# Performance work log

Measured on AMD Instinct MI355X. Metric: run time of the kernel, lower is better.

The kernel has to match this reference:

```python
import jax, jax.numpy as jnp
import numpy as np
import math

NUM_HEADS = 16

def setup_inputs() -> dict:
    key = jax.random.key(0)
    ks = jax.random.split(key, 5)
    d_model = 1024
    std = math.sqrt(2.0 / (d_model + d_model))
    x = jax.random.normal(ks[0], (2, 2048, d_model), dtype=jnp.float32)
    Wq = jax.random.normal(ks[1], (d_model, d_model), dtype=jnp.float32) * std
    Wk = jax.random.normal(ks[2], (d_model, d_model), dtype=jnp.float32) * std
    Wv = jax.random.normal(ks[3], (d_model, d_model), dtype=jnp.float32) * std
    Wo = jax.random.normal(ks[4], (d_model, d_model), dtype=jnp.float32) * std
    return {"x": x, "Wq": Wq, "Wk": Wk, "Wv": Wv, "Wo": Wo}

def reference(x, Wq, Wk, Wv, Wo):
    # x: [b, s, d]; W*: [d_out, d_in]
    b, s, d = x.shape
    h = NUM_HEADS
    dh = d // h
    def proj(W):
        y = jnp.einsum('bsd,ed->bse', x, W)           # [b, s, d]
        return y.reshape(b, s, h, dh).transpose(0, 2, 1, 3)  # [b, h, s, dh]
    Q, K, V = proj(Wq), proj(Wk), proj(Wv)
    scale = 1.0 / math.sqrt(dh)
    logits = jnp.einsum('bhqd,bhkd->bhqk', Q, K) * scale  # [b, h, s, s]
    causal = jnp.tril(jnp.ones((s, s), dtype=bool))
    logits = jnp.where(causal, logits, -jnp.inf)
    attn = jax.nn.softmax(logits, axis=-1)
    out = jnp.einsum('bhqk,bhkd->bhqd', attn, V)          # [b, h, s, dh]
    out = out.transpose(0, 2, 1, 3).reshape(b, s, d)
    return jnp.einsum('bsv,dv->bsd', out, Wo)
```

## Files before the change

kernel.cpp:

```cpp
#include <hip/hip_runtime.h>
#include <hip/hip_bf16.h>
#include <math.h>

typedef unsigned short ushort_t;
typedef __attribute__((ext_vector_type(8))) short bf16x8;
typedef __attribute__((ext_vector_type(4))) float f32x4;

#define MFMA16(a,b,c) __builtin_amdgcn_mfma_f32_16x16x32_bf16(a,b,c,0,0,0)
#define QSCALE 0.1803368801111204f

typedef unsigned int u32;
typedef __attribute__((address_space(1))) const u32* gp1_t;
typedef __attribute__((address_space(3))) u32* lp3_t;

__device__ __forceinline__ void async_copy16(void* l, const void* g) {
    __builtin_amdgcn_global_load_lds((gp1_t)g, (lp3_t)l, 16, 0, 0);
}

__device__ __forceinline__ ushort_t f2bf(float f) {
    unsigned u = __float_as_uint(f);
    unsigned r = u + 0x7fffu + ((u >> 16) & 1u);
    return (ushort_t)(r >> 16);
}

__global__ __launch_bounds__(256) void cvt_kernel(
    const float* __restrict__ x,  const float* __restrict__ wq,
    const float* __restrict__ wk, const float* __restrict__ wv,
    const float* __restrict__ wo, ushort_t* __restrict__ dst)
{
    size_t base = ((size_t)blockIdx.x * 256 + threadIdx.x) * 8;
    const float* src; size_t off;
    if      (base < 4194304ul) { src = x;  off = base; }
    else if (base < 5242880ul) { src = wq; off = base - 4194304ul; }
    else if (base < 6291456ul) { src = wk; off = base - 5242880ul; }
    else if (base < 7340032ul) { src = wv; off = base - 6291456ul; }
    else                       { src = wo; off = base - 7340032ul; }
    float4 a = *(const float4*)(src + off);
    float4 b = *(const float4*)(src + off + 4);
    struct alignas(16) U8 { ushort_t v[8]; } o;
    o.v[0]=f2bf(a.x); o.v[1]=f2bf(a.y); o.v[2]=f2bf(a.z); o.v[3]=f2bf(a.w);
    o.v[4]=f2bf(b.x); o.v[5]=f2bf(b.y); o.v[6]=f2bf(b.z); o.v[7]=f2bf(b.w);
    *(U8*)(dst + base) = o;
}

__global__ __launch_bounds__(512) void gemm_bt(
    const ushort_t* __restrict__ A, const ushort_t* __restrict__ B,
    ushort_t* __restrict__ Oq, ushort_t* __restrict__ Ok,
    ushort_t* __restrict__ Ovt, float* __restrict__ Of, int is_out)
{
    __shared__ ushort_t As[2][128 * 64];
    __shared__ ushort_t Bs[2][128 * 64];
    const int t = threadIdx.x, l = t & 63, w = t >> 6;
    const int l4 = l >> 4, lm = l & 15;
    const int wr = w >> 1, wc = w & 1;

    const int nwg = gridDim.x * gridDim.y;
    const int orig = (int)blockIdx.y * gridDim.x + (int)blockIdx.x;
    const int qq = nwg >> 3;
    const int swz = (orig & 7) * qq + (orig >> 3);
    const int n0 = (swz % gridDim.x) * 128;
    const int m0 = (swz / gridDim.x) * 128;

    const int srow = t >> 3, scol = t & 7;

    f32x4 acc[2][4] = {};

    #pragma unroll
    for (int i = 0; i < 2; ++i) {
        const int row = i * 64 + srow;
        const int c = scol ^ (row & 7);
        async_copy16((char*)&As[0][0] + i * 8192 + t * 16,
                     A + (size_t)(m0 + row) * 1024 + c * 8);
        async_copy16((char*)&Bs[0][0] + i * 8192 + t * 16,
                     B + (size_t)(n0 + row) * 1024 + c * 8);
    }

    for (int kt = 0; kt < 16; ++kt) {
        const int cur = kt & 1;
        if (kt + 1 < 16) {
            const int k0 = (kt + 1) * 64;
            #pragma unroll
            for (int i = 0; i < 2; ++i) {
                const int row = i * 64 + srow;
                const int c = scol ^ (row & 7);
                async_copy16((char*)&As[cur ^ 1][0] + i * 8192 + t * 16,
                             A + (size_t)(m0 + row) * 1024 + k0 + c * 8);
                async_copy16((char*)&Bs[cur ^ 1][0] + i * 8192 + t * 16,
                             B + (size_t)(n0 + row) * 1024 + k0 + c * 8);
            }
            asm volatile("s_waitcnt vmcnt(4)" ::: "memory");
        } else {
            asm volatile("s_waitcnt vmcnt(0)" ::: "memory");
        }
        __builtin_amdgcn_s_barrier();

        #pragma unroll
        for (int ks = 0; ks < 2; ++ks) {
            bf16x8 af[2], bfr[4];
            #pragma unroll
            for (int mi = 0; mi < 2; ++mi) {
                const int row = wr * 32 + mi * 16 + lm;
                const int ch = l4 + 4 * ks;
                af[mi] = *(const bf16x8*)(&As[cur][0] + row * 64 + ((ch ^ (row & 7)) << 3));
            }
            #pragma unroll
            for (int ni = 0; ni < 4; ++ni) {
                const int row = wc * 64 + ni * 16 + lm;
                const int ch = l4 + 4 * ks;
                bfr[ni] = *(const bf16x8*)(&Bs[cur][0] + row * 64 + ((ch ^ (row & 7)) << 3));
            }
            #pragma unroll
            for (int mi = 0; mi < 2; ++mi)
                #pragma unroll
                for (int ni = 0; ni < 4; ++ni)
                    acc[mi][ni] = MFMA16(af[mi], bfr[ni], acc[mi][ni]);
        }
        asm volatile("s_waitcnt lgkmcnt(0)" ::: "memory");
        __builtin_amdgcn_s_barrier();
    }

    const int mb = m0 + wr * 32, nb = n0 + wc * 64;
    if (is_out) {
        #pragma unroll
        for (int mi = 0; mi < 2; ++mi)
            #pragma unroll
            for (int ni = 0; ni < 4; ++ni) {
                const int n = nb + ni * 16 + lm;
                const int mr = mb + mi * 16 + l4 * 4;
                #pragma unroll
                for (int r = 0; r < 4; ++r)
                    Of[(size_t)(mr + r) * 1024 + n] = acc[mi][ni][r];
            }
    } else if (nb >= 2048) {
        #pragma unroll
        for (int mi = 0; mi < 2; ++mi)
            #pragma unroll
            for (int ni = 0; ni < 4; ++ni) {
                const int nv = nb - 2048 + ni * 16 + lm;
                const int m = mb + mi * 16 + l4 * 4;
                const int b = m >> 11, s = m & 2047, h = nv >> 6, d = nv & 63;
                ushort4 pk;
                pk.x = f2bf(acc[mi][ni][0]); pk.y = f2bf(acc[mi][ni][1]);
                pk.z = f2bf(acc[mi][ni][2]); pk.w = f2bf(acc[mi][ni][3]);
                *(ushort4*)(Ovt + (((size_t)(b * 16 + h) * 64 + d) * 2048 + s)) = pk;
            }
    } else {
        ushort_t* O = (nb < 1024) ? Oq : Ok;
        const float qs = (nb < 1024) ? (float)QSCALE : 1.0f;
        const int nbase = nb & 1023;
        #pragma unroll
        for (int mi = 0; mi < 2; ++mi)
            #pragma unroll
            for (int ni = 0; ni < 4; ++ni) {
                const int n = nbase + ni * 16 + lm;
                const int h = n >> 6, d = n & 63;
                #pragma unroll
                for (int r = 0; r < 4; ++r) {
                    const int m = mb + mi * 16 + l4 * 4 + r;
                    const int b = m >> 11, s = m & 2047;
                    O[((size_t)(b * 16 + h) * 2048 + s) * 64 + d] =
                        f2bf(acc[mi][ni][r] * qs);
                }
            }
    }
}

template<bool MASK>
__device__ __forceinline__ void attn_tile2(
    const ushort_t* Kbuf, const ushort_t* Vbuf, ushort_t* Pw,
    const bf16x8 (&qf)[2][2], const bf16x8 ones,
    f32x4 (&o)[2][4], f32x4 (&ol)[2],
    int kv0, int q0w, int l4, int lm)
{
    f32x4 sf[2][4] = {};
    #pragma unroll
    for (int ks = 0; ks < 2; ++ks)
        #pragma unroll
        for (int cf = 0; cf < 4; ++cf) {
            const int rowK = cf * 16 + lm;
            const int ch = l4 + 4 * ks;
            bf16x8 kf = *(const bf16x8*)(Kbuf + rowK * 64 + ((ch ^ (rowK & 7)) << 3));
            sf[0][cf] = MFMA16(kf, qf[0][ks], sf[0][cf]);
            sf[1][cf] = MFMA16(kf, qf[1][ks], sf[1][cf]);
        }

    #pragma unroll
    for (int qi = 0; qi < 2; ++qi) {
        const int qrow = q0w + qi * 16 + lm;
        #pragma unroll
        for (int cf = 0; cf < 4; ++cf) {
            f32x4 s = sf[qi][cf];
            if (MASK) {
                #pragma unroll
                for (int r = 0; r < 4; ++r)
                    if (kv0 + cf * 16 + l4 * 4 + r > qrow) s[r] = -30000.f;
            }
            float p0 = __builtin_amdgcn_exp2f(s[0]);
            float p1 = __builtin_amdgcn_exp2f(s[1]);
            float p2 = __builtin_amdgcn_exp2f(s[2]);
            float p3 = __builtin_amdgcn_exp2f(s[3]);
            __hip_bfloat162 b01 = __float22bfloat162_rn(make_float2(p0, p1));
            __hip_bfloat162 b23 = __float22bfloat162_rn(make_float2(p2, p3));
            uint2 pkv;
            __builtin_memcpy(&pkv.x, &b01, 4);
            __builtin_memcpy(&pkv.y, &b23, 4);
            *(uint2*)&Pw[(qi * 16 + lm) * 72 + cf * 16 + l4 * 4] = pkv;
        }
    }

    #pragma unroll
    for (int ks = 0; ks < 2; ++ks) {
        bf16x8 pf0 = *(const bf16x8*)&Pw[(0 * 16 + lm) * 72 + ks * 32 + l4 * 8];
        bf16x8 pf1 = *(const bf16x8*)&Pw[(1 * 16 + lm) * 72 + ks * 32 + l4 * 8];
        #pragma unroll
        for (int df = 0; df < 4; ++df) {
            const int rowV = df * 16 + lm;
            const int ch = l4 + 4 * ks;
            bf16x8 vf = *(const bf16x8*)(Vbuf + rowV * 64 + ((ch ^ (rowV & 7)) << 3));
            o[0][df] = MFMA16(vf, pf0, o[0][df]);
            o[1][df] = MFMA16(vf, pf1, o[1][df]);
        }
        ol[0] = MFMA16(ones, pf0, ol[0]);
        ol[1] = MFMA16(ones, pf1, ol[1]);
    }
}

__global__ __launch_bounds__(512) void attn_kernel(
    const ushort_t* __restrict__ Qg, const ushort_t* __restrict__ Kg,
    const ushort_t* __restrict__ Vtg, ushort_t* __restrict__ Og)
{
    __shared__ ushort_t smem[51200];
    ushort_t* Ksm = smem;
    ushort_t* Vsm = smem + 16384;
    ushort_t* Psm = smem + 32768;

    const int t = threadIdx.x, l = t & 63, w = t >> 6;
    const int l4 = l >> 4, lm = l & 15;
    const int kvg = w >> 2, qg = w & 3;
    const int bh = blockIdx.x;
    const int qt = 15 - (int)blockIdx.y;
    const int q0 = qt * 128, q0w = q0 + qg * 32;

    const ushort_t* Kbh = Kg + (size_t)bh * 2048 * 64;
    const ushort_t* Vbh = Vtg + (size_t)bh * 64 * 2048;

    bf16x8 qf[2][2];
    #pragma unroll
    for (int qi = 0; qi < 2; ++qi) {
        const ushort_t* qp = Qg + ((size_t)bh * 2048 + q0w + qi * 16 + lm) * 64 + l4 * 8;
        qf[qi][0] = *(const bf16x8*)qp;
        qf[qi][1] = *(const bf16x8*)(qp + 32);
    }
    bf16x8 ones;
    #pragma unroll
    for (int i = 0; i < 8; ++i) ones[i] = (short)0x3F80;

    f32x4 o[2][4] = {};
    f32x4 ol[2] = {};

    const int tg = t & 255;
    const int sr0 = tg >> 3, sc0 = tg & 7;
    const ushort_t* kp[2]; const ushort_t* vp[2];
    char* kd[2]; char* vd[2];
    #pragma unroll
    for (int i = 0; i < 2; ++i) {
        const int row = i * 32 + sr0;
        const int c = sc0 ^ (row & 7);
        kp[i] = Kbh + row * 64 + c * 8;
        vp[i] = Vbh + (size_t)row * 2048 + c * 8;
        kd[i] = (char*)Ksm + kvg * 16384 + i * 4096 + tg * 16;
        vd[i] = (char*)Vsm + kvg * 16384 + i * 4096 + tg * 16;
    }
    ushort_t* Pw = Psm + w * 2304;
    const ushort_t* Kgrp = Ksm + kvg * 8192;
    const ushort_t* Vgrp = Vsm + kvg * 8192;

    const int nst = qt + 1;
    {
        const int kv0p = kvg * 64;
        #pragma unroll
        for (int i = 0; i < 2; ++i) {
            async_copy16(kd[i], kp[i] + (size_t)kv0p * 64);
            async_copy16(vd[i], vp[i] + kv0p);
        }
    }

    for (int s = 0; s < nst; ++s) {
        const int cur = s & 1;
        if (s + 1 < nst) {
            const int kv0n = (2 * (s + 1) + kvg) * 64;
            #pragma unroll
            for (int i = 0; i < 2; ++i) {
                async_copy16(kd[i] + (cur ^ 1) * 8192, kp[i] + (size_t)kv0n * 64);
                async_copy16(vd[i] + (cur ^ 1) * 8192, vp[i] + kv0n);
            }
            asm volatile("s_waitcnt vmcnt(4)" ::: "memory");
        } else {
            asm volatile("s_waitcnt vmcnt(0)" ::: "memory");
        }
        __builtin_amdgcn_s_barrier();

        const int kv0 = (2 * s + kvg) * 64;
        if ((s + 1 < nst) || (q0w + 31 >= kv0)) {
            if (s + 1 < nst)
                attn_tile2<false>(Kgrp + cur * 4096, Vgrp + cur * 4096, Pw,
                                  qf, ones, o, ol, kv0, q0w, l4, lm);
            else
                attn_tile2<true>(Kgrp + cur * 4096, Vgrp + cur * 4096, Pw,
                                 qf, ones, o, ol, kv0, q0w, l4, lm);
        }
        asm volatile("s_waitcnt lgkmcnt(0)" ::: "memory");
        __builtin_amdgcn_s_barrier();
    }

    float* sc = (float*)smem;
    const int mb_ = (qg * 64 + l) * 35;
    if (kvg == 1) {
        #pragma unroll
        for (int qi = 0; qi < 2; ++qi) {
            #pragma unroll
            for (int df = 0; df < 4; ++df)
                #pragma unroll
                for (int r = 0; r < 4; ++r)
                    sc[mb_ + qi * 17 + df * 4 + r] = o[qi][df][r];
            sc[mb_ + qi * 17 + 16] = ol[qi][0];
        }
    }
    __syncthreads();
    if (kvg == 0) {
        const int b = bh >> 4, h = bh & 15;
        #pragma unroll
        for (int qi = 0; qi < 2; ++qi) {
            const float lB = sc[mb_ + qi * 17 + 16];
            const float inv = 1.f / (ol[qi][0] + lB);
            const int srow_o = q0w + qi * 16 + lm;
            #pragma unroll
            for (int df = 0; df < 4; ++df) {
                ushort4 pk4;
                float v0 = (o[qi][df][0] + sc[mb_ + qi * 17 + df * 4 + 0]) * inv;
                float v1 = (o[qi][df][1] + sc[mb_ + qi * 17 + df * 4 + 1]) * inv;
                float v2 = (o[qi][df][2] + sc[mb_ + qi * 17 + df * 4 + 2]) * inv;
                float v3 = (o[qi][df][3] + sc[mb_ + qi * 17 + df * 4 + 3]) * inv;
                pk4.x = f2bf(v0); pk4.y = f2bf(v1); pk4.z = f2bf(v2); pk4.w = f2bf(v3);
                *(ushort4*)&Og[((size_t)(b * 2048 + srow_o)) * 1024 + h * 64 + df * 16 + l4 * 4] = pk4;
            }
        }
    }
}

extern "C" void kernel_launch(void* const* d_in, const int* in_sizes, int n_in,
                              void* d_out, int out_size, void* d_ws, size_t ws_size,
                              hipStream_t stream)
{
    const float* x  = (const float*)d_in[0];
    const float* Wq = (const float*)d_in[1];
    const float* Wk = (const float*)d_in[2];
    const float* Wv = (const float*)d_in[3];
    const float* Wo = (const float*)d_in[4];

    ushort_t* ws  = (ushort_t*)d_ws;
    ushort_t* xb  = ws;
    ushort_t* wqb = ws + 4194304;
    ushort_t* wob = ws + 7340032;
    ushort_t* Qw  = ws + 8388608;
    ushort_t* Kw  = ws + 12582912;
    ushort_t* Vtw = ws + 16777216;
    ushort_t* Aow = ws + 20971520;

    cvt_kernel<<<4096, 256, 0, stream>>>(x, Wq, Wk, Wv, Wo, ws);
    gemm_bt<<<dim3(24, 32), 512, 0, stream>>>(xb, wqb, Qw, Kw, Vtw, nullptr, 0);
    attn_kernel<<<dim3(32, 16), 512, 0, stream>>>(Qw, Kw, Vtw, Aow);
    gemm_bt<<<dim3(8, 32), 512, 0, stream>>>(Aow, wob, nullptr, nullptr, nullptr,
                                             (float*)d_out, 1);
}
```

Before: 101.5 us.

## Single-buffer V loads inside the step and split P buffer per query half

```diff
diff --git a/kernel.cpp b/kernel.cpp
--- a/kernel.cpp
+++ b/kernel.cpp
@@ -165,81 +165,18 @@
     }
 }
 
-template<bool MASK>
-__device__ __forceinline__ void attn_tile2(
-    const ushort_t* Kbuf, const ushort_t* Vbuf, ushort_t* Pw,
-    const bf16x8 (&qf)[2][2], const bf16x8 ones,
-    f32x4 (&o)[2][4], f32x4 (&ol)[2],
-    int kv0, int q0w, int l4, int lm)
-{
-    f32x4 sf[2][4] = {};
-    #pragma unroll
-    for (int ks = 0; ks < 2; ++ks)
-        #pragma unroll
-        for (int cf = 0; cf < 4; ++cf) {
-            const int rowK = cf * 16 + lm;
-            const int ch = l4 + 4 * ks;
-            bf16x8 kf = *(const bf16x8*)(Kbuf + rowK * 64 + ((ch ^ (rowK & 7)) << 3));
-            sf[0][cf] = MFMA16(kf, qf[0][ks], sf[0][cf]);
-            sf[1][cf] = MFMA16(kf, qf[1][ks], sf[1][cf]);
-        }
-
-    #pragma unroll
-    for (int qi = 0; qi < 2; ++qi) {
-        const int qrow = q0w + qi * 16 + lm;
-        #pragma unroll
-        for (int cf = 0; cf < 4; ++cf) {
-            f32x4 s = sf[qi][cf];
-            if (MASK) {
-                #pragma unroll
-                for (int r = 0; r < 4; ++r)
-                    if (kv0 + cf * 16 + l4 * 4 + r > qrow) s[r] = -30000.f;
-            }
-            float p0 = __builtin_amdgcn_exp2f(s[0]);
-            float p1 = __builtin_amdgcn_exp2f(s[1]);
-            float p2 = __builtin_amdgcn_exp2f(s[2]);
-            float p3 = __builtin_amdgcn_exp2f(s[3]);
-            __hip_bfloat162 b01 = __float22bfloat162_rn(make_float2(p0, p1));
-            __hip_bfloat162 b23 = __float22bfloat162_rn(make_float2(p2, p3));
-            uint2 pkv;
-            __builtin_memcpy(&pkv.x, &b01, 4);
-            __builtin_memcpy(&pkv.y, &b23, 4);
-            *(uint2*)&Pw[(qi * 16 + lm) * 72 + cf * 16 + l4 * 4] = pkv;
-        }
-    }
-
-    #pragma unroll
-    for (int ks = 0; ks < 2; ++ks) {
-        bf16x8 pf0 = *(const bf16x8*)&Pw[(0 * 16 + lm) * 72 + ks * 32 + l4 * 8];
-        bf16x8 pf1 = *(const bf16x8*)&Pw[(1 * 16 + lm) * 72 + ks * 32 + l4 * 8];
-        #pragma unroll
-        for (int df = 0; df < 4; ++df) {
-            const int rowV = df * 16 + lm;
-            const int ch = l4 + 4 * ks;
-            bf16x8 vf = *(const bf16x8*)(Vbuf + rowV * 64 + ((ch ^ (rowV & 7)) << 3));
-            o[0][df] = MFMA16(vf, pf0, o[0][df]);
-            o[1][df] = MFMA16(vf, pf1, o[1][df]);
-        }
-        ol[0] = MFMA16(ones, pf0, ol[0]);
-        ol[1] = MFMA16(ones, pf1, ol[1]);
-    }
-}
-
 __global__ __launch_bounds__(512) void attn_kernel(
     const ushort_t* __restrict__ Qg, const ushort_t* __restrict__ Kg,
     const ushort_t* __restrict__ Vtg, ushort_t* __restrict__ Og)
 {
-    __shared__ ushort_t smem[51200];
-    ushort_t* Ksm = smem;
-    ushort_t* Vsm = smem + 16384;
-    ushort_t* Psm = smem + 32768;
+    __shared__ char smem[65536];
 
     const int t = threadIdx.x, l = t & 63, w = t >> 6;
     const int l4 = l >> 4, lm = l & 15;
     const int kvg = w >> 2, qg = w & 3;
     const int bh = blockIdx.x;
     const int qt = 15 - (int)blockIdx.y;
-    const int q0 = qt * 128, q0w = q0 + qg * 32;
+    const int q0w = qt * 128 + qg * 32;
 
     const ushort_t* Kbh = Kg + (size_t)bh * 2048 * 64;
     const ushort_t* Vbh = Vtg + (size_t)bh * 64 * 2048;
@@ -268,46 +205,132 @@
         const int c = sc0 ^ (row & 7);
         kp[i] = Kbh + row * 64 + c * 8;
         vp[i] = Vbh + (size_t)row * 2048 + c * 8;
-        kd[i] = (char*)Ksm + kvg * 16384 + i * 4096 + tg * 16;
-        vd[i] = (char*)Vsm + kvg * 16384 + i * 4096 + tg * 16;
-    }
-    ushort_t* Pw = Psm + w * 2304;
-    const ushort_t* Kgrp = Ksm + kvg * 8192;
-    const ushort_t* Vgrp = Vsm + kvg * 8192;
+        kd[i] = smem + kvg * 16384 + i * 4096 + tg * 16;
+        vd[i] = smem + 32768 + kvg * 8192 + i * 4096 + tg * 16;
+    }
+    const int pswz = (lm & 7) << 4;
+    char* Pw = smem + 49152 + w * 2048;
+    const ushort_t* Vgrp = (const ushort_t*)(smem + 32768 + kvg * 8192);
 
     const int nst = qt + 1;
     {
         const int kv0p = kvg * 64;
         #pragma unroll
-        for (int i = 0; i < 2; ++i) {
+        for (int i = 0; i < 2; ++i)
             async_copy16(kd[i], kp[i] + (size_t)kv0p * 64);
-            async_copy16(vd[i], vp[i] + kv0p);
-        }
     }
 
     for (int s = 0; s < nst; ++s) {
         const int cur = s & 1;
+        const int kv0 = (2 * s + kvg) * 64;
+        #pragma unroll
+        for (int i = 0; i < 2; ++i)
+            async_copy16(vd[i], vp[i] + kv0);
         if (s + 1 < nst) {
             const int kv0n = (2 * (s + 1) + kvg) * 64;
             #pragma unroll
-            for (int i = 0; i < 2; ++i) {
+            for (int i = 0; i < 2; ++i)
                 async_copy16(kd[i] + (cur ^ 1) * 8192, kp[i] + (size_t)kv0n * 64);
-                async_copy16(vd[i] + (cur ^ 1) * 8192, vp[i] + kv0n);
-            }
             asm volatile("s_waitcnt vmcnt(4)" ::: "memory");
         } else {
-            asm volatile("s_waitcnt vmcnt(0)" ::: "memory");
-        }
-        __builtin_amdgcn_s_barrier();
-
-        const int kv0 = (2 * s + kvg) * 64;
-        if ((s + 1 < nst) || (q0w + 31 >= kv0)) {
-            if (s + 1 < nst)
-                attn_tile2<false>(Kgrp + cur * 4096, Vgrp + cur * 4096, Pw,
-                                  qf, ones, o, ol, kv0, q0w, l4, lm);
-            else
-                attn_tile2<true>(Kgrp + cur * 4096, Vgrp + cur * 4096, Pw,
-                                 qf, ones, o, ol, kv0, q0w, l4, lm);
+            asm volatile("s_waitcnt vmcnt(2)" ::: "memory");
+        }
+        __builtin_amdgcn_s_barrier();
+
+        const bool active = (s + 1 < nst) || (q0w + 31 >= kv0);
+        const bool last = (s + 1 == nst);
+        const ushort_t* Kgrp = (const ushort_t*)(smem + kvg * 16384 + cur * 8192);
+
+        f32x4 sf[2][4];
+        if (active) {
+            #pragma unroll
+            for (int qi = 0; qi < 2; ++qi)
+                #pragma unroll
+                for (int cf = 0; cf < 4; ++cf) sf[qi][cf] = (f32x4){0,0,0,0};
+            #pragma unroll
+            for (int ks = 0; ks < 2; ++ks)
+                #pragma unroll
+                for (int cf = 0; cf < 4; ++cf) {
+                    const int rowK = cf * 16 + lm;
+                    const int ch = l4 + 4 * ks;
+                    bf16x8 kf = *(const bf16x8*)(Kgrp + rowK * 64 + ((ch ^ (rowK & 7)) << 3));
+                    sf[0][cf] = MFMA16(kf, qf[0][ks], sf[0][cf]);
+                    sf[1][cf] = MFMA16(kf, qf[1][ks], sf[1][cf]);
+                }
+            {
+                const int qrow = q0w + 0 * 16 + lm;
+                #pragma unroll
+                for (int cf = 0; cf < 4; ++cf) {
+                    f32x4 sv = sf[0][cf];
+                    if (last) {
+                        #pragma unroll
+                        for (int r = 0; r < 4; ++r)
+                            if (kv0 + cf * 16 + l4 * 4 + r > qrow) sv[r] = -30000.f;
+                    }
+                    float p0 = __builtin_amdgcn_exp2f(sv[0]);
+                    float p1 = __builtin_amdgcn_exp2f(sv[1]);
+                    float p2 = __builtin_amdgcn_exp2f(sv[2]);
+                    float p3 = __builtin_amdgcn_exp2f(sv[3]);
+                    __hip_bfloat162 b01 = __float22bfloat162_rn(make_float2(p0, p1));
+                    __hip_bfloat162 b23 = __float22bfloat162_rn(make_float2(p2, p3));
+                    uint2 pkv;
+                    __builtin_memcpy(&pkv.x, &b01, 4);
+                    __builtin_memcpy(&pkv.y, &b23, 4);
+                    *(uint2*)(Pw + ((lm * 128 + cf * 32 + l4 * 8) ^ pswz)) = pkv;
+                }
+            }
+        }
+        asm volatile("s_waitcnt vmcnt(2)" ::: "memory");
+        if (last) asm volatile("s_waitcnt vmcnt(0)" ::: "memory");
+        __builtin_amdgcn_s_barrier();
+
+        if (active) {
+            #pragma unroll
+            for (int ks = 0; ks < 2; ++ks) {
+                bf16x8 pf = *(const bf16x8*)(Pw + ((lm * 128 + ks * 64 + l4 * 16) ^ pswz));
+                #pragma unroll
+                for (int df = 0; df < 4; ++df) {
+                    const int rowV = df * 16 + lm;
+                    const int ch = l4 + 4 * ks;
+                    bf16x8 vf = *(const bf16x8*)(Vgrp + rowV * 64 + ((ch ^ (rowV & 7)) << 3));
+                    o[0][df] = MFMA16(vf, pf, o[0][df]);
+                }
+                ol[0] = MFMA16(ones, pf, ol[0]);
+            }
+            {
+                const int qrow = q0w + 1 * 16 + lm;
+                #pragma unroll
+                for (int cf = 0; cf < 4; ++cf) {
+                    f32x4 sv = sf[1][cf];
+                    if (last) {
+                        #pragma unroll
+                        for (int r = 0; r < 4; ++r)
+                            if (kv0 + cf * 16 + l4 * 4 + r > qrow) sv[r] = -30000.f;
+                    }
+                    float p0 = __builtin_amdgcn_exp2f(sv[0]);
+                    float p1 = __builtin_amdgcn_exp2f(sv[1]);
+                    float p2 = __builtin_amdgcn_exp2f(sv[2]);
+                    float p3 = __builtin_amdgcn_exp2f(sv[3]);
+                    __hip_bfloat162 b01 = __float22bfloat162_rn(make_float2(p0, p1));
+                    __hip_bfloat162 b23 = __float22bfloat162_rn(make_float2(p2, p3));
+                    uint2 pkv;
+                    __builtin_memcpy(&pkv.x, &b01, 4);
+                    __builtin_memcpy(&pkv.y, &b23, 4);
+                    *(uint2*)(Pw + ((lm * 128 + cf * 32 + l4 * 8) ^ pswz)) = pkv;
+                }
+            }
+            #pragma unroll
+            for (int ks = 0; ks < 2; ++ks) {
+                bf16x8 pf = *(const bf16x8*)(Pw + ((lm * 128 + ks * 64 + l4 * 16) ^ pswz));
+                #pragma unroll
+                for (int df = 0; df < 4; ++df) {
+                    const int rowV = df * 16 + lm;
+                    const int ch = l4 + 4 * ks;
+                    bf16x8 vf = *(const bf16x8*)(Vgrp + rowV * 64 + ((ch ^ (rowV & 7)) << 3));
+                    o[1][df] = MFMA16(vf, pf, o[1][df]);
+                }
+                ol[1] = MFMA16(ones, pf, ol[1]);
+            }
         }
         asm volatile("s_waitcnt lgkmcnt(0)" ::: "memory");
         __builtin_amdgcn_s_barrier();
```

Result: no change. 101.4 us (-0.2%).
